# Optimization experiments

Measured on AMD Instinct MI355X. Metric: run time of the kernel, lower is better.

The kernel has to match this reference:

```python
import jax, jax.numpy as jnp
import numpy as np
from jax import lax

# hyperparameters (match init_kwargs)
N_INP, N_HID, N_OUT = 3, 64, 10
SEQ_LEN, N_ROLL, K = 8, 16, 3
DT, GAMMA, EPS = 0.042, 2.7, 4.7
H, W = 12, 10            # hard-coded in coRNNCell2's PixelwiseConv2d
PAD = (K - 1) // 2
BATCH = 16


def setup_inputs() -> dict:
    key = jax.random.key(0)
    ks = jax.random.split(key, 7)
    x = jax.random.normal(ks[0], (SEQ_LEN, BATCH, N_INP, H, W), dtype=jnp.float32)
    # readin: Conv2d(seq_len*n_inp -> 2*n_hid, k, padding=1, replicate)
    readin_w = jax.random.normal(ks[1], (2 * N_HID, SEQ_LEN * N_INP, K, K), dtype=jnp.float32) * 0.05
    readin_b = jax.random.normal(ks[2], (2 * N_HID,), dtype=jnp.float32) * 0.05
    # PixelwiseConv2d: per-output-pixel weights (out, in, k, k, H, W)
    pw_w = jax.random.normal(ks[3], (N_HID, 2 * N_HID, K, K, H, W), dtype=jnp.float32) * 0.05
    pw_b = jax.random.normal(ks[4], (N_HID, H, W), dtype=jnp.float32) * 0.05
    # readout: 1x1 conv (n_hid -> n_out)
    readout_w = jax.random.normal(ks[5], (N_OUT, N_HID), dtype=jnp.float32) * 0.05
    readout_b = jax.random.normal(ks[6], (N_OUT,), dtype=jnp.float32) * 0.05
    return {"x": x, "readin_w": readin_w, "readin_b": readin_b,
            "pw_w": pw_w, "pw_b": pw_b,
            "readout_w": readout_w, "readout_b": readout_b}


def _pixelwise_conv(x, pw_w, pw_b):
    # x: (B, 2*N_HID, H, W); zero padding like F.unfold(padding=PAD)
    B = x.shape[0]
    xp = jnp.pad(x, ((0, 0), (0, 0), (PAD, PAD), (PAD, PAD)))
    # patches ordered (c, i, j) to match unfold().view(B, C, k, k, H, W)
    patches = jnp.stack([xp[:, :, i:i + H, j:j + W]
                         for i in range(K) for j in range(K)], axis=2)
    patches = patches.reshape(B, 2 * N_HID, K, K, H, W)
    return jnp.einsum('bcijhw,ocijhw->bohw', patches, pw_w) + pw_b[None]


def reference(x, readin_w, readin_b, pw_w, pw_b, readout_w, readout_b):
    T, B = x.shape[0], x.shape[1]
    # 't b c h w -> b (t c) h w'
    xr = jnp.transpose(x, (1, 0, 2, 3, 4)).reshape(B, T * N_INP, H, W)
    # readin conv with replicate padding
    xr_p = jnp.pad(xr, ((0, 0), (0, 0), (PAD, PAD), (PAD, PAD)), mode='edge')
    h = lax.conv_general_dilated(xr_p, readin_w, (1, 1), 'VALID',
                                 dimension_numbers=('NCHW', 'OIHW', 'NCHW'))
    h = h + readin_b[None, :, None, None]
    hy, hz = h[:, :N_HID], h[:, N_HID:]

    def step(carry, _):
        hy, hz = carry
        pre = _pixelwise_conv(jnp.concatenate([hz, hy], axis=1), pw_w, pw_b)
        hz = hz + DT * (jnp.tanh(pre) - GAMMA * hy - EPS * hz)
        hy = hy + DT * hz
        return (hy, hz), None

    (hy, hz), _ = lax.scan(step, (hy, hz), None, length=N_ROLL)
    out = jnp.einsum('bchw,oc->bohw', hy, readout_w) + readout_b[None, :, None, None]
    return out
```

## Files before the change

kernel.cpp:

```cpp
#include <hip/hip_runtime.h>
#include <hip/hip_cooperative_groups.h>
#include <math.h>

#define N_INPC 3
#define N_HID 64
#define N_OUTC 10
#define SEQ_LEN 8
#define N_ROLL 16
#define DT 0.042f
#define GAMMA 2.7f
#define EPSC 4.7f
#define HH 12
#define WW 10
#define NPIX 120
#define BATCH 16
#define NC 128
#define NK 1152

typedef __attribute__((ext_vector_type(8))) short short8;
typedef __attribute__((ext_vector_type(4))) float f32x4;
typedef unsigned short ushort_t;
typedef unsigned long long u64;

__device__ __forceinline__ ushort_t f2bf(float v) {
  union { float f; unsigned u; } x; x.f = v;
  unsigned r = x.u + 0x7fff + ((x.u >> 16) & 1);
  return (ushort_t)(r >> 16);
}

__global__ __launch_bounds__(256) void transpose2_kernel(
    const float* __restrict__ pw_w, ushort_t* __restrict__ Wt) {
  const int t = blockIdx.x * 256 + threadIdx.x;
  if (t >= 120 * 9216) return;
  const int p = t % 120;
  const int rest = t / 120;
  const int o = rest & 15;
  const int kg = (rest >> 4) & 3;
  const int ks = (rest >> 6) % 36;
  const int hot = (rest >> 6) / 36;
  const int o_g = (hot >> 1) * 32 + (hot & 1) * 16 + o;
  const int k0 = ks * 32 + kg * 8;
  ushort_t out8[8];
#pragma unroll
  for (int j = 0; j < 8; ++j) {
    const int kp = k0 + j;
    const int ij = kp >> 7;
    const int c = kp & 127;
    out8[j] = f2bf(pw_w[((size_t)o_g * NK + c * 9 + ij) * NPIX + p]);
  }
  uint4 pack;
  pack.x = (unsigned)out8[0] | ((unsigned)out8[1] << 16);
  pack.y = (unsigned)out8[2] | ((unsigned)out8[3] << 16);
  pack.z = (unsigned)out8[4] | ((unsigned)out8[5] << 16);
  pack.w = (unsigned)out8[6] | ((unsigned)out8[7] << 16);
  *(uint4*)(Wt + ((size_t)p * 9216 + rest) * 8) = pack;
}

__global__ __launch_bounds__(256) void readin2_kernel(
    const float* __restrict__ x, const float* __restrict__ rw,
    const float* __restrict__ rb, float* __restrict__ Sm,
    ushort_t* __restrict__ Sg) {
  const int n = blockIdx.x * 256 + threadIdx.x;
  if (n >= BATCH * NC * NPIX) return;
  const int p = n % NPIX;
  const int oc = (n / NPIX) & 127;
  const int b = n / (NPIX * NC);
  const int ph = p / WW, pw_ = p % WW;
  float acc = rb[oc];
  for (int ch = 0; ch < SEQ_LEN * N_INPC; ++ch) {
    const int tt = ch / N_INPC, ic = ch % N_INPC;
    const float* xb = x + (((tt * BATCH + b) * N_INPC + ic) * HH) * WW;
    const float* wb = rw + (oc * (SEQ_LEN * N_INPC) + ch) * 9;
#pragma unroll
    for (int di = 0; di < 3; ++di) {
      int ih = ph + di - 1;
      ih = ih < 0 ? 0 : (ih > HH - 1 ? HH - 1 : ih);
#pragma unroll
      for (int dj = 0; dj < 3; ++dj) {
        int iw = pw_ + dj - 1;
        iw = iw < 0 ? 0 : (iw > WW - 1 ? WW - 1 : iw);
        acc += xb[ih * WW + iw] * wb[di * 3 + dj];
      }
    }
  }
  const int sc = (oc < 64) ? (64 + oc) : (oc - 64);
  const size_t idx = ((size_t)(p * BATCH + b)) * NC + sc;
  Sm[idx] = acc;
  Sg[idx] = f2bf(acc);
}

__global__ __launch_bounds__(256, 1) void persist5_kernel(
    const ushort_t* __restrict__ Wt, ushort_t* __restrict__ SgA,
    ushort_t* __restrict__ SgB, float* __restrict__ Sm,
    const float* __restrict__ pwb, int* __restrict__ flags) {
  __shared__ short8 SA[2304];
  __shared__ f32x4 red[128];
  __shared__ ushort_t tmp[16][64];
  const int wg = blockIdx.x, p = wg >> 1, h = wg & 1;
  const int ph = p / WW, pw_ = p % WW;
  const int tid = threadIdx.x, wv = tid >> 6, l = tid & 63;
  const int ot = wv & 1, kq = wv >> 1;
  const int kg = l >> 4, c16 = l & 15;
  const int o_g = h * 32 + ot * 16 + c16;

  bool relevant = false;
  int faddr = 0;
  if (wv == 0 && l < 18) {
    const int q = l >> 1;
    const int nh = ph + q / 3 - 1, nw = pw_ + q % 3 - 1;
    if ((unsigned)nh < (unsigned)HH && (unsigned)nw < (unsigned)WW) {
      relevant = true;
      faddr = (((nh * WW + nw) << 1) | (l & 1)) * 16;
    }
  }

  short8 breg[18];
  {
    const short8* __restrict__ WB =
        (const short8*)Wt + ((size_t)((p * 2 + h) * 2 + ot)) * 2304 + kg * 16 + c16;
#pragma unroll
    for (int j = 0; j < 18; ++j) breg[j] = WB[(size_t)(kq * 18 + j) * 64];
  }
  const float pb = pwb[o_g * NPIX + p];

  const int b0 = (l >> 4) * 4;
  float hzr[4], hyr[4];
  if (wv < 2) {
#pragma unroll
    for (int r = 0; r < 4; ++r) {
      const size_t iz = ((size_t)(p * BATCH + b0 + r)) * NC + o_g;
      hzr[r] = Sm[iz];
      hyr[r] = Sm[iz + 64];
    }
  }

  const int ab = tid >> 4, am = tid & 15;
  const int abm = ab * NC + am * 8;

  for (int s = 0; s < N_ROLL; ++s) {
    const ushort_t* __restrict__ sgc = (s & 1) ? SgB : SgA;
    ushort_t* __restrict__ sgn = (s & 1) ? SgA : SgB;

    if (s > 0) {
      if (wv == 0) {
        while (true) {
          int f = 0x7fffffff;
          if (relevant)
            f = __hip_atomic_load(flags + faddr, __ATOMIC_RELAXED,
                                  __HIP_MEMORY_SCOPE_AGENT);
          if (__all(!relevant || f >= s)) break;
          __builtin_amdgcn_s_sleep(1);
        }
      }
      __syncthreads();
    }

#pragma unroll
    for (int q = 0; q < 9; ++q) {
      const int ih = ph + q / 3 - 1, iw = pw_ + q % 3 - 1;
      union { u64 u[2]; short8 s8; } cv;
      cv.u[0] = 0; cv.u[1] = 0;
      if ((unsigned)ih < (unsigned)HH && (unsigned)iw < (unsigned)WW) {
        const u64* src =
            (const u64*)(sgc + (size_t)(ih * WW + iw) * (BATCH * NC) + abm);
        cv.u[0] = __hip_atomic_load(src, __ATOMIC_RELAXED,
                                    __HIP_MEMORY_SCOPE_AGENT);
        cv.u[1] = __hip_atomic_load(src + 1, __ATOMIC_RELAXED,
                                    __HIP_MEMORY_SCOPE_AGENT);
      }
      const int row = q * 16 + am;
      SA[row * 16 + (ab ^ am)] = cv.s8;
    }
    __syncthreads();

    f32x4 acc0 = {0.f, 0.f, 0.f, 0.f}, acc1 = {0.f, 0.f, 0.f, 0.f};
#pragma unroll
    for (int ii = 0; ii < 9; ++ii) {
      const int ks0 = kq * 18 + ii * 2;
      {
        const int row = ks0 * 4 + kg;
        acc0 = __builtin_amdgcn_mfma_f32_16x16x32_bf16(
            SA[row * 16 + (c16 ^ (row & 15))], breg[ii * 2], acc0, 0, 0, 0);
      }
      {
        const int row = (ks0 + 1) * 4 + kg;
        acc1 = __builtin_amdgcn_mfma_f32_16x16x32_bf16(
            SA[row * 16 + (c16 ^ (row & 15))], breg[ii * 2 + 1], acc1, 0, 0, 0);
      }
    }
    f32x4 acc = acc0 + acc1;

    if (wv >= 2) red[(wv - 2) * 64 + l] = acc;
    __syncthreads();
    if (wv < 2) {
      acc += red[wv * 64 + l];
#pragma unroll
      for (int r = 0; r < 4; ++r) {
        const float pre = acc[r] + pb;
        const float hz = hzr[r], hy = hyr[r];
        const float hzn = hz + DT * (tanhf(pre) - GAMMA * hy - EPSC * hz);
        const float hyn = hy + DT * hzn;
        hzr[r] = hzn;
        hyr[r] = hyn;
        tmp[b0 + r][ot * 16 + c16] = f2bf(hzn);
        tmp[b0 + r][32 + ot * 16 + c16] = f2bf(hyn);
      }
    }

    if (s < N_ROLL - 1) {
      __syncthreads();
      {
        const int b = tid >> 4, zy = (tid >> 3) & 1, g = tid & 7;
        union { ushort_t us[4]; u64 u; } pk;
#pragma unroll
        for (int j = 0; j < 4; ++j) pk.us[j] = tmp[b][zy * 32 + g * 4 + j];
        u64* dst = (u64*)(sgn + (size_t)(p * BATCH + b) * NC + zy * 64 +
                          h * 32 + g * 4);
        __hip_atomic_store(dst, pk.u, __ATOMIC_RELAXED,
                           __HIP_MEMORY_SCOPE_AGENT);
      }
      __syncthreads();
      if (tid == 0)
        __hip_atomic_store(flags + wg * 16, s + 1, __ATOMIC_RELAXED,
                           __HIP_MEMORY_SCOPE_AGENT);
    }
  }

  if (wv < 2) {
#pragma unroll
    for (int r = 0; r < 4; ++r) {
      const size_t iz = ((size_t)(p * BATCH + b0 + r)) * NC + o_g;
      Sm[iz] = hzr[r];
      Sm[iz + 64] = hyr[r];
    }
  }
}

__global__ __launch_bounds__(256) void readout2_kernel(
    const float* __restrict__ Sm, const float* __restrict__ row,
    const float* __restrict__ rob, float* __restrict__ out) {
  const int n = blockIdx.x * 256 + threadIdx.x;
  if (n >= BATCH * N_OUTC * NPIX) return;
  const int p = n % NPIX;
  const int o = (n / NPIX) % N_OUTC;
  const int b = n / (NPIX * N_OUTC);
  float acc = rob[o];
  const float* hy = Sm + ((size_t)(p * BATCH + b)) * NC + 64;
#pragma unroll 8
  for (int c = 0; c < 64; ++c) acc += hy[c] * row[o * 64 + c];
  out[n] = acc;
}

extern "C" void kernel_launch(void* const* d_in, const int* in_sizes, int n_in,
                              void* d_out, int out_size, void* d_ws, size_t ws_size,
                              hipStream_t stream) {
  const float* x         = (const float*)d_in[0];
  const float* readin_w  = (const float*)d_in[1];
  const float* readin_b  = (const float*)d_in[2];
  const float* pw_w      = (const float*)d_in[3];
  const float* pw_b      = (const float*)d_in[4];
  const float* readout_w = (const float*)d_in[5];
  const float* readout_b = (const float*)d_in[6];
  float* out = (float*)d_out;

  ushort_t* Wt  = (ushort_t*)d_ws;
  ushort_t* Sg0 = Wt + (size_t)120 * 9216 * 8;
  ushort_t* Sg1 = Sg0 + 245760;
  float*    Sm0 = (float*)(Sg1 + 245760);
  int*      flg = (int*)(Sm0 + 245760);

  transpose2_kernel<<<4320, 256, 0, stream>>>(pw_w, Wt);
  readin2_kernel<<<(BATCH * NC * NPIX + 255) / 256, 256, 0, stream>>>(
      x, readin_w, readin_b, Sm0, Sg0);

  {
    const ushort_t* aWt = Wt;
    ushort_t* aSgA = Sg0;
    ushort_t* aSgB = Sg1;
    float* aSm = Sm0;
    const float* aPwb = pw_b;
    int* aFlg = flg;
    void* args[] = {(void*)&aWt, (void*)&aSgA, (void*)&aSgB,
                    (void*)&aSm, (void*)&aPwb, (void*)&aFlg};
    hipLaunchCooperativeKernel((const void*)persist5_kernel, dim3(NPIX * 2),
                               dim3(256), args, 0, stream);
  }

  readout2_kernel<<<(BATCH * N_OUTC * NPIX + 255) / 256, 256, 0, stream>>>(
      Sm0, readout_w, readout_b, out);
}
```

Before: 216.8 us.

## Fuse readin and readout into persistent kernel with one block per pixel

Merges the readin convolution and the readout projection into the persistent cooperative kernel, removing two separate launches and the float state round-trip through global memory. Each pixel is now handled by one 512-thread block covering all 64 hidden outputs instead of two 256-thread blocks. This halves the number of flags each block polls and lets the centre-pixel tap come from local shared memory. The cost is redundant readin work per block and a larger block on one CU. There is also a new step-0 flag wait, which relies on stale flags from earlier runs not being misread.

```diff
diff --git a/kernel.cpp b/kernel.cpp
--- a/kernel.cpp
+++ b/kernel.cpp
@@ -1,5 +1,4 @@
 #include <hip/hip_runtime.h>
-#include <hip/hip_cooperative_groups.h>
 #include <math.h>
 
 #define N_INPC 3
@@ -37,8 +36,8 @@
   const int o = rest & 15;
   const int kg = (rest >> 4) & 3;
   const int ks = (rest >> 6) % 36;
-  const int hot = (rest >> 6) / 36;
-  const int o_g = (hot >> 1) * 32 + (hot & 1) * 16 + o;
+  const int T = (rest >> 6) / 36;
+  const int o_g = T * 16 + o;
   const int k0 = ks * 32 + kg * 8;
   ushort_t out8[8];
 #pragma unroll
@@ -56,120 +55,155 @@
   *(uint4*)(Wt + ((size_t)p * 9216 + rest) * 8) = pack;
 }
 
-__global__ __launch_bounds__(256) void readin2_kernel(
-    const float* __restrict__ x, const float* __restrict__ rw,
-    const float* __restrict__ rb, float* __restrict__ Sm,
-    ushort_t* __restrict__ Sg) {
-  const int n = blockIdx.x * 256 + threadIdx.x;
-  if (n >= BATCH * NC * NPIX) return;
-  const int p = n % NPIX;
-  const int oc = (n / NPIX) & 127;
-  const int b = n / (NPIX * NC);
-  const int ph = p / WW, pw_ = p % WW;
-  float acc = rb[oc];
-  for (int ch = 0; ch < SEQ_LEN * N_INPC; ++ch) {
-    const int tt = ch / N_INPC, ic = ch % N_INPC;
-    const float* xb = x + (((tt * BATCH + b) * N_INPC + ic) * HH) * WW;
-    const float* wb = rw + (oc * (SEQ_LEN * N_INPC) + ch) * 9;
-#pragma unroll
-    for (int di = 0; di < 3; ++di) {
-      int ih = ph + di - 1;
-      ih = ih < 0 ? 0 : (ih > HH - 1 ? HH - 1 : ih);
-#pragma unroll
-      for (int dj = 0; dj < 3; ++dj) {
-        int iw = pw_ + dj - 1;
-        iw = iw < 0 ? 0 : (iw > WW - 1 ? WW - 1 : iw);
-        acc += xb[ih * WW + iw] * wb[di * 3 + dj];
-      }
-    }
-  }
-  const int sc = (oc < 64) ? (64 + oc) : (oc - 64);
-  const size_t idx = ((size_t)(p * BATCH + b)) * NC + sc;
-  Sm[idx] = acc;
-  Sg[idx] = f2bf(acc);
-}
-
-__global__ __launch_bounds__(256, 1) void persist5_kernel(
+__global__ __launch_bounds__(512, 1) void persist6_kernel(
     const ushort_t* __restrict__ Wt, ushort_t* __restrict__ SgA,
-    ushort_t* __restrict__ SgB, float* __restrict__ Sm,
-    const float* __restrict__ pwb, int* __restrict__ flags) {
-  __shared__ short8 SA[2304];
-  __shared__ f32x4 red[128];
-  __shared__ ushort_t tmp[16][64];
-  const int wg = blockIdx.x, p = wg >> 1, h = wg & 1;
+    ushort_t* __restrict__ SgB, const float* __restrict__ x,
+    const float* __restrict__ rw, const float* __restrict__ rb,
+    const float* __restrict__ pwb, const float* __restrict__ row,
+    const float* __restrict__ rob, float* __restrict__ out,
+    int* __restrict__ flags) {
+  __shared__ char shraw[36864] __attribute__((aligned(16)));
+  short8* SA = (short8*)shraw;
+  float (*Sf)[128] = (float(*)[128])shraw;
+  float (*hyf)[64] = (float(*)[64])shraw;
+  __shared__ f32x4 red[256];
+  __shared__ ushort_t tmp[16][128];
+
+  const int p = blockIdx.x;
   const int ph = p / WW, pw_ = p % WW;
   const int tid = threadIdx.x, wv = tid >> 6, l = tid & 63;
-  const int ot = wv & 1, kq = wv >> 1;
+  const int ot = wv & 3, kq = wv >> 2;
   const int kg = l >> 4, c16 = l & 15;
-  const int o_g = h * 32 + ot * 16 + c16;
+  const int o_g = ot * 16 + c16;
+  const int b0 = (l >> 4) * 4;
 
   bool relevant = false;
   int faddr = 0;
-  if (wv == 0 && l < 18) {
-    const int q = l >> 1;
+  if (wv == 0 && l < 8) {
+    const int q = l + (l >= 4);
     const int nh = ph + q / 3 - 1, nw = pw_ + q % 3 - 1;
     if ((unsigned)nh < (unsigned)HH && (unsigned)nw < (unsigned)WW) {
       relevant = true;
-      faddr = (((nh * WW + nw) << 1) | (l & 1)) * 16;
-    }
-  }
+      faddr = (nh * WW + nw) * 16;
+    }
+  }
+
+  {
+    const int c = tid & 127;
+    const int bq = tid >> 7;
+    const int oc = (c < 64) ? (64 + c) : (c - 64);
+    int ihs[3], iws[3];
+#pragma unroll
+    for (int d = 0; d < 3; ++d) {
+      int ih = ph + d - 1; ihs[d] = ih < 0 ? 0 : (ih > HH - 1 ? HH - 1 : ih);
+      int iw = pw_ + d - 1; iws[d] = iw < 0 ? 0 : (iw > WW - 1 ? WW - 1 : iw);
+    }
+    float a[4];
+#pragma unroll
+    for (int j = 0; j < 4; ++j) a[j] = rb[oc];
+    for (int ch = 0; ch < SEQ_LEN * N_INPC; ++ch) {
+      const int tt = ch / N_INPC, ic = ch % N_INPC;
+      const float* wb = rw + (oc * (SEQ_LEN * N_INPC) + ch) * 9;
+      float w9[9];
+#pragma unroll
+      for (int t2 = 0; t2 < 9; ++t2) w9[t2] = wb[t2];
+#pragma unroll
+      for (int j = 0; j < 4; ++j) {
+        const float* xb =
+            x + (((size_t)(tt * BATCH + bq * 4 + j) * N_INPC + ic) * HH) * WW;
+        float s = 0.f;
+#pragma unroll
+        for (int di = 0; di < 3; ++di)
+#pragma unroll
+          for (int dj = 0; dj < 3; ++dj)
+            s += xb[ihs[di] * WW + iws[dj]] * w9[di * 3 + dj];
+        a[j] += s;
+      }
+    }
+#pragma unroll
+    for (int j = 0; j < 4; ++j) Sf[bq * 4 + j][c] = a[j];
+  }
+  __syncthreads();
+
+  float hzr[4], hyr[4];
+  if (wv < 4) {
+#pragma unroll
+    for (int r = 0; r < 4; ++r) {
+      hzr[r] = Sf[b0 + r][o_g];
+      hyr[r] = Sf[b0 + r][64 + o_g];
+      tmp[b0 + r][o_g] = f2bf(hzr[r]);
+      tmp[b0 + r][64 + o_g] = f2bf(hyr[r]);
+    }
+  }
+  __syncthreads();
+
+  {
+    const int b = tid >> 5, ci = tid & 31;
+    union { ushort_t us[4]; u64 u; } pk;
+#pragma unroll
+    for (int j2 = 0; j2 < 4; ++j2) pk.us[j2] = tmp[b][ci * 4 + j2];
+    u64* dst = (u64*)(SgA + ((size_t)(p * BATCH + b)) * NC + ci * 4);
+    __hip_atomic_store(dst, pk.u, __ATOMIC_RELAXED, __HIP_MEMORY_SCOPE_AGENT);
+  }
+  __syncthreads();
+  if (tid == 0)
+    __hip_atomic_store(flags + p * 16, 0, __ATOMIC_RELAXED,
+                       __HIP_MEMORY_SCOPE_AGENT);
 
   short8 breg[18];
   {
     const short8* __restrict__ WB =
-        (const short8*)Wt + ((size_t)((p * 2 + h) * 2 + ot)) * 2304 + kg * 16 + c16;
+        (const short8*)Wt + ((size_t)(p * 4 + ot)) * 2304 + kg * 16 + c16;
 #pragma unroll
     for (int j = 0; j < 18; ++j) breg[j] = WB[(size_t)(kq * 18 + j) * 64];
   }
   const float pb = pwb[o_g * NPIX + p];
 
-  const int b0 = (l >> 4) * 4;
-  float hzr[4], hyr[4];
-  if (wv < 2) {
-#pragma unroll
-    for (int r = 0; r < 4; ++r) {
-      const size_t iz = ((size_t)(p * BATCH + b0 + r)) * NC + o_g;
-      hzr[r] = Sm[iz];
-      hyr[r] = Sm[iz + 64];
-    }
-  }
-
-  const int ab = tid >> 4, am = tid & 15;
-  const int abm = ab * NC + am * 8;
+  const int half = tid >> 8;
+  const int hb = (tid >> 4) & 15;
+  const int m = tid & 15;
+  const int bm = hb * NC + m * 8;
 
   for (int s = 0; s < N_ROLL; ++s) {
     const ushort_t* __restrict__ sgc = (s & 1) ? SgB : SgA;
     ushort_t* __restrict__ sgn = (s & 1) ? SgA : SgB;
 
-    if (s > 0) {
-      if (wv == 0) {
-        while (true) {
-          int f = 0x7fffffff;
-          if (relevant)
-            f = __hip_atomic_load(flags + faddr, __ATOMIC_RELAXED,
-                                  __HIP_MEMORY_SCOPE_AGENT);
-          if (__all(!relevant || f >= s)) break;
-          __builtin_amdgcn_s_sleep(1);
+    if (wv == 0) {
+      while (true) {
+        int f = 0x7fffffff;
+        if (relevant)
+          f = __hip_atomic_load(flags + faddr, __ATOMIC_RELAXED,
+                                __HIP_MEMORY_SCOPE_AGENT);
+        if (__all(!relevant || f >= s)) break;
+        __builtin_amdgcn_s_sleep(1);
+      }
+    }
+    __syncthreads();
+
+#pragma unroll
+    for (int i = 0; i < 5; ++i) {
+      if (half == 0 || i < 4) {
+        const int q = 2 * i + half;
+        short8 v;
+        if (half == 0 && i == 2) {
+          v = *(const short8*)&tmp[hb][m * 8];
+        } else {
+          const int ih = ph + q / 3 - 1, iw = pw_ + q % 3 - 1;
+          union { u64 u[2]; short8 s8; } cv;
+          cv.u[0] = 0; cv.u[1] = 0;
+          if ((unsigned)ih < (unsigned)HH && (unsigned)iw < (unsigned)WW) {
+            const u64* src =
+                (const u64*)(sgc + (size_t)(ih * WW + iw) * (BATCH * NC) + bm);
+            cv.u[0] = __hip_atomic_load(src, __ATOMIC_RELAXED,
+                                        __HIP_MEMORY_SCOPE_AGENT);
+            cv.u[1] = __hip_atomic_load(src + 1, __ATOMIC_RELAXED,
+                                        __HIP_MEMORY_SCOPE_AGENT);
+          }
+          v = cv.s8;
         }
-      }
-      __syncthreads();
-    }
-
-#pragma unroll
-    for (int q = 0; q < 9; ++q) {
-      const int ih = ph + q / 3 - 1, iw = pw_ + q % 3 - 1;
-      union { u64 u[2]; short8 s8; } cv;
-      cv.u[0] = 0; cv.u[1] = 0;
-      if ((unsigned)ih < (unsigned)HH && (unsigned)iw < (unsigned)WW) {
-        const u64* src =
-            (const u64*)(sgc + (size_t)(ih * WW + iw) * (BATCH * NC) + abm);
-        cv.u[0] = __hip_atomic_load(src, __ATOMIC_RELAXED,
-                                    __HIP_MEMORY_SCOPE_AGENT);
-        cv.u[1] = __hip_atomic_load(src + 1, __ATOMIC_RELAXED,
-                                    __HIP_MEMORY_SCOPE_AGENT);
-      }
-      const int row = q * 16 + am;
-      SA[row * 16 + (ab ^ am)] = cv.s8;
+        const int rw_ = q * 16 + m;
+        SA[rw_ * 16 + (hb ^ m)] = v;
+      }
     }
     __syncthreads();
 
@@ -178,21 +212,21 @@
     for (int ii = 0; ii < 9; ++ii) {
       const int ks0 = kq * 18 + ii * 2;
       {
-        const int row = ks0 * 4 + kg;
+        const int r_ = ks0 * 4 + kg;
         acc0 = __builtin_amdgcn_mfma_f32_16x16x32_bf16(
-            SA[row * 16 + (c16 ^ (row & 15))], breg[ii * 2], acc0, 0, 0, 0);
+            SA[r_ * 16 + (c16 ^ (r_ & 15))], breg[ii * 2], acc0, 0, 0, 0);
       }
       {
-        const int row = (ks0 + 1) * 4 + kg;
+        const int r_ = (ks0 + 1) * 4 + kg;
         acc1 = __builtin_amdgcn_mfma_f32_16x16x32_bf16(
-            SA[row * 16 + (c16 ^ (row & 15))], breg[ii * 2 + 1], acc1, 0, 0, 0);
+            SA[r_ * 16 + (c16 ^ (r_ & 15))], breg[ii * 2 + 1], acc1, 0, 0, 0);
       }
     }
     f32x4 acc = acc0 + acc1;
 
-    if (wv >= 2) red[(wv - 2) * 64 + l] = acc;
+    if (wv >= 4) red[(wv - 4) * 64 + l] = acc;
     __syncthreads();
-    if (wv < 2) {
+    if (wv < 4) {
       acc += red[wv * 64 + l];
 #pragma unroll
       for (int r = 0; r < 4; ++r) {
@@ -202,53 +236,44 @@
         const float hyn = hy + DT * hzn;
         hzr[r] = hzn;
         hyr[r] = hyn;
-        tmp[b0 + r][ot * 16 + c16] = f2bf(hzn);
-        tmp[b0 + r][32 + ot * 16 + c16] = f2bf(hyn);
+        if (s < N_ROLL - 1) {
+          tmp[b0 + r][o_g] = f2bf(hzn);
+          tmp[b0 + r][64 + o_g] = f2bf(hyn);
+        }
       }
     }
 
     if (s < N_ROLL - 1) {
       __syncthreads();
       {
-        const int b = tid >> 4, zy = (tid >> 3) & 1, g = tid & 7;
+        const int b = tid >> 5, ci = tid & 31;
         union { ushort_t us[4]; u64 u; } pk;
 #pragma unroll
-        for (int j = 0; j < 4; ++j) pk.us[j] = tmp[b][zy * 32 + g * 4 + j];
-        u64* dst = (u64*)(sgn + (size_t)(p * BATCH + b) * NC + zy * 64 +
-                          h * 32 + g * 4);
+        for (int j2 = 0; j2 < 4; ++j2) pk.us[j2] = tmp[b][ci * 4 + j2];
+        u64* dst = (u64*)(sgn + ((size_t)(p * BATCH + b)) * NC + ci * 4);
         __hip_atomic_store(dst, pk.u, __ATOMIC_RELAXED,
                            __HIP_MEMORY_SCOPE_AGENT);
       }
       __syncthreads();
       if (tid == 0)
-        __hip_atomic_store(flags + wg * 16, s + 1, __ATOMIC_RELAXED,
+        __hip_atomic_store(flags + p * 16, s + 1, __ATOMIC_RELAXED,
                            __HIP_MEMORY_SCOPE_AGENT);
     }
   }
 
-  if (wv < 2) {
-#pragma unroll
-    for (int r = 0; r < 4; ++r) {
-      const size_t iz = ((size_t)(p * BATCH + b0 + r)) * NC + o_g;
-      Sm[iz] = hzr[r];
-      Sm[iz + 64] = hyr[r];
-    }
-  }
-}
-
-__global__ __launch_bounds__(256) void readout2_kernel(
-    const float* __restrict__ Sm, const float* __restrict__ row,
-    const float* __restrict__ rob, float* __restrict__ out) {
-  const int n = blockIdx.x * 256 + threadIdx.x;
-  if (n >= BATCH * N_OUTC * NPIX) return;
-  const int p = n % NPIX;
-  const int o = (n / NPIX) % N_OUTC;
-  const int b = n / (NPIX * N_OUTC);
-  float acc = rob[o];
-  const float* hy = Sm + ((size_t)(p * BATCH + b)) * NC + 64;
+  __syncthreads();
+  if (wv < 4) {
+#pragma unroll
+    for (int r = 0; r < 4; ++r) hyf[b0 + r][o_g] = hyr[r];
+  }
+  __syncthreads();
+  if (tid < BATCH * N_OUTC) {
+    const int b = tid / N_OUTC, o = tid % N_OUTC;
+    float acc2 = rob[o];
 #pragma unroll 8
-  for (int c = 0; c < 64; ++c) acc += hy[c] * row[o * 64 + c];
-  out[n] = acc;
+    for (int c2 = 0; c2 < 64; ++c2) acc2 += hyf[b][c2] * row[o * 64 + c2];
+    out[((size_t)(b * N_OUTC + o)) * NPIX + p] = acc2;
+  }
 }
 
 extern "C" void kernel_launch(void* const* d_in, const int* in_sizes, int n_in,
@@ -266,26 +291,26 @@
   ushort_t* Wt  = (ushort_t*)d_ws;
   ushort_t* Sg0 = Wt + (size_t)120 * 9216 * 8;
   ushort_t* Sg1 = Sg0 + 245760;
-  float*    Sm0 = (float*)(Sg1 + 245760);
-  int*      flg = (int*)(Sm0 + 245760);
+  int*      flg = (int*)(Sg1 + 245760);
 
   transpose2_kernel<<<4320, 256, 0, stream>>>(pw_w, Wt);
-  readin2_kernel<<<(BATCH * NC * NPIX + 255) / 256, 256, 0, stream>>>(
-      x, readin_w, readin_b, Sm0, Sg0);
 
   {
     const ushort_t* aWt = Wt;
     ushort_t* aSgA = Sg0;
     ushort_t* aSgB = Sg1;
-    float* aSm = Sm0;
+    const float* aX = x;
+    const float* aRw = readin_w;
+    const float* aRb = readin_b;
     const float* aPwb = pw_b;
+    const float* aRow = readout_w;
+    const float* aRob = readout_b;
+    float* aOut = out;
     int* aFlg = flg;
-    void* args[] = {(void*)&aWt, (void*)&aSgA, (void*)&aSgB,
-                    (void*)&aSm, (void*)&aPwb, (void*)&aFlg};
-    hipLaunchCooperativeKernel((const void*)persist5_kernel, dim3(NPIX * 2),
-                               dim3(256), args, 0, stream);
-  }
-
-  readout2_kernel<<<(BATCH * N_OUTC * NPIX + 255) / 256, 256, 0, stream>>>(
-      Sm0, readout_w, readout_b, out);
+    void* args[] = {(void*)&aWt, (void*)&aSgA, (void*)&aSgB, (void*)&aX,
+                    (void*)&aRw, (void*)&aRb,  (void*)&aPwb, (void*)&aRow,
+                    (void*)&aRob, (void*)&aOut, (void*)&aFlg};
+    hipLaunchCooperativeKernel((const void*)persist6_kernel, dim3(NPIX),
+                               dim3(512), args, 0, stream);
+  }
 }
```

Result: faster. 202.2 us (-6.8%).
